# Kernel optimization log

Hardware: AMD Instinct MI355X
Metric: run time of the kernel (lower is better)

Reference implementation:

```python
import jax, jax.numpy as jnp
import numpy as np
import math

VOCAB = 32000
D_MODEL = 1024
N_HEADS = 16
D_FF = 4096
N_LAYERS = 4
MAX_LEN = 2048
BATCH = 2
SEQ = 1024


def _sinusoidal_pe(max_len, d_model):
    pos = np.arange(max_len, dtype=np.float32)[:, None]
    div = np.exp(np.arange(0, d_model, 2, dtype=np.float32) * (-math.log(10000.0) / d_model))
    pe = np.zeros((max_len, d_model), dtype=np.float32)
    pe[:, 0::2] = np.sin(pos * div)
    pe[:, 1::2] = np.cos(pos * div)
    return jnp.asarray(pe)


def setup_inputs() -> dict:
    key = jax.random.key(0)
    ks = jax.random.split(key, 16)
    std = 0.02
    L, d, ff, V = N_LAYERS, D_MODEL, D_FF, VOCAB
    inp = {
        "input_ids": jax.random.randint(ks[0], (BATCH, SEQ), 0, V, dtype=jnp.int32),
        "tok_emb": jax.random.normal(ks[1], (V, d), jnp.float32) * std,
        "pe": _sinusoidal_pe(MAX_LEN, d),
        "Wq": jax.random.normal(ks[2], (L, d, d), jnp.float32) * std,
        "Wk": jax.random.normal(ks[3], (L, d, d), jnp.float32) * std,
        "Wv": jax.random.normal(ks[4], (L, d, d), jnp.float32) * std,
        "Wo": jax.random.normal(ks[5], (L, d, d), jnp.float32) * std,
        "bo": jnp.zeros((L, d), jnp.float32),
        "W1": jax.random.normal(ks[6], (L, d, ff), jnp.float32) * std,
        "b1": jnp.zeros((L, ff), jnp.float32),
        "W2": jax.random.normal(ks[7], (L, ff, d), jnp.float32) * std,
        "b2": jnp.zeros((L, d), jnp.float32),
        "ln1_g": jnp.ones((L, d), jnp.float32),
        "ln1_b": jnp.zeros((L, d), jnp.float32),
        "ln2_g": jnp.ones((L, d), jnp.float32),
        "ln2_b": jnp.zeros((L, d), jnp.float32),
        "lnf_g": jnp.ones((d,), jnp.float32),
        "lnf_b": jnp.zeros((d,), jnp.float32),
        "Whead": jax.random.normal(ks[8], (V, d), jnp.float32) * std,
    }
    return inp


def _layernorm(x, g, b, eps=1e-5):
    mu = jnp.mean(x, axis=-1, keepdims=True)
    var = jnp.var(x, axis=-1, keepdims=True)
    return (x - mu) * jax.lax.rsqrt(var + eps) * g + b


def reference(input_ids, tok_emb, pe, Wq, Wk, Wv, Wo, bo, W1, b1, W2, b2,
              ln1_g, ln1_b, ln2_g, ln2_b, lnf_g, lnf_b, Whead):
    B, S = input_ids.shape
    d, H = D_MODEL, N_HEADS
    dk = d // H
    scale = math.sqrt(dk)

    x = tok_emb[input_ids] * math.sqrt(d) + pe[:S][None, :, :]  # [B,S,d]
    causal = jnp.tril(jnp.ones((S, S), dtype=bool))  # [S,S]

    for l in range(N_LAYERS):
        # --- attention sub-block (pre-LN) ---
        h = _layernorm(x, ln1_g[l], ln1_b[l])
        q = (h @ Wq[l]).reshape(B, S, H, dk).transpose(0, 2, 1, 3)  # [B,H,S,dk]
        k = (h @ Wk[l]).reshape(B, S, H, dk).transpose(0, 2, 1, 3)
        v = (h @ Wv[l]).reshape(B, S, H, dk).transpose(0, 2, 1, 3)
        scores = jnp.einsum('bhqd,bhkd->bhqk', q, k) / scale  # [B,H,S,S]
        scores = jnp.where(causal[None, None], scores, -1e9)
        attn = jax.nn.softmax(scores, axis=-1)
        ctx = jnp.einsum('bhqk,bhkd->bhqd', attn, v)  # [B,H,S,dk]
        ctx = ctx.transpose(0, 2, 1, 3).reshape(B, S, d)
        x = x + ctx @ Wo[l] + bo[l]
        # --- feed-forward sub-block ---
        h = _layernorm(x, ln2_g[l], ln2_b[l])
        x = x + jax.nn.relu(h @ W1[l] + b1[l]) @ W2[l] + b2[l]

    x = _layernorm(x, lnf_g, lnf_b)
    logits = x @ Whead.T  # [B,S,V]
    return logits
```

## Files before the change

### kernel.cpp

```cpp
#include <hip/hip_runtime.h>
#include <stdint.h>

typedef unsigned short u16;
typedef unsigned int   u32;

#define D_MODEL 1024
#define NHEADS  16
#define DKH     64
#define DFF     4096
#define NLAYERS 4
#define BATCH   2
#define SEQ     1024
#define NTOK    (BATCH*SEQ)
#define NVOCAB  32000
#define QKV_LD  3072

typedef __bf16 bf16x8 __attribute__((ext_vector_type(8)));
typedef float  f32x4  __attribute__((ext_vector_type(4)));
typedef u32    u32x4  __attribute__((ext_vector_type(4)));

static __device__ __forceinline__ u16 f2bf(float f){
    union { float f; u32 u; } v; v.f = f;
    return (u16)((v.u + 0x7fffu + ((v.u >> 16) & 1u)) >> 16);
}
static __device__ __forceinline__ u32 pk2(float lo, float hi){
    return (u32)f2bf(lo) | ((u32)f2bf(hi) << 16);
}
static __device__ __forceinline__ bf16x8 ldb8(const u16* p){
    return *reinterpret_cast<const bf16x8*>(p);
}
static __device__ __forceinline__ f32x4 mfma16(bf16x8 a, bf16x8 b, f32x4 c){
    return __builtin_amdgcn_mfma_f32_16x16x32_bf16(a, b, c, 0, 0, 0);
}
static __device__ __forceinline__ void gld16(const void* g, void* l){
    __builtin_amdgcn_global_load_lds((__attribute__((address_space(1))) u32*)g,
                                     (__attribute__((address_space(3))) u32*)l, 16, 0, 0);
}

__global__ __launch_bounds__(256) void k_embed(const int* __restrict__ ids,
        const float* __restrict__ tok, const float* __restrict__ pe,
        float* __restrict__ x){
    int t = blockIdx.x;
    int c = threadIdx.x * 4;
    int id = ids[t];
    int s = t & (SEQ - 1);
    float4 tv = *(const float4*)(tok + (size_t)id * D_MODEL + c);
    float4 pv = *(const float4*)(pe  + (size_t)s  * D_MODEL + c);
    float4 o;
    o.x = tv.x * 32.0f + pv.x;
    o.y = tv.y * 32.0f + pv.y;
    o.z = tv.z * 32.0f + pv.z;
    o.w = tv.w * 32.0f + pv.w;
    *(float4*)(x + (size_t)t * D_MODEL + c) = o;
}

__global__ __launch_bounds__(256) void k_ln(const float* __restrict__ x,
        const float* __restrict__ g, const float* __restrict__ b,
        u16* __restrict__ out){
    int t = blockIdx.x;
    int tid = threadIdx.x;
    float4 v = *(const float4*)(x + (size_t)t * D_MODEL + tid * 4);
    float s  = v.x + v.y + v.z + v.w;
    float ss = v.x*v.x + v.y*v.y + v.z*v.z + v.w*v.w;
    #pragma unroll
    for (int off = 1; off < 64; off <<= 1){
        s  += __shfl_xor(s, off);
        ss += __shfl_xor(ss, off);
    }
    __shared__ float rs[4], rss[4];
    int w = tid >> 6;
    if ((tid & 63) == 0){ rs[w] = s; rss[w] = ss; }
    __syncthreads();
    s  = rs[0] + rs[1] + rs[2] + rs[3];
    ss = rss[0] + rss[1] + rss[2] + rss[3];
    float mu  = s * (1.0f / D_MODEL);
    float var = ss * (1.0f / D_MODEL) - mu * mu;
    float rstd = rsqrtf(var + 1e-5f);
    float4 gg = *(const float4*)(g + tid * 4);
    float4 bb = *(const float4*)(b + tid * 4);
    uint2 pkv;
    pkv.x = pk2((v.x - mu) * rstd * gg.x + bb.x, (v.y - mu) * rstd * gg.y + bb.y);
    pkv.y = pk2((v.z - mu) * rstd * gg.z + bb.z, (v.w - mu) * rstd * gg.w + bb.w);
    *(uint2*)(out + (size_t)t * D_MODEL + tid * 4) = pkv;
}

__global__ __launch_bounds__(256) void k_ln_acc(float* __restrict__ x,
        const float* __restrict__ p0, const float* __restrict__ p1,
        const float* __restrict__ bias,
        const float* __restrict__ g, const float* __restrict__ b,
        u16* __restrict__ out){
    int t = blockIdx.x;
    int tid = threadIdx.x;
    size_t idx = (size_t)t * D_MODEL + tid * 4;
    float4 v  = *(const float4*)(x + idx);
    float4 a0 = *(const float4*)(p0 + idx);
    float4 a1 = *(const float4*)(p1 + idx);
    float4 bv = *(const float4*)(bias + tid * 4);
    v.x += a0.x + a1.x + bv.x;
    v.y += a0.y + a1.y + bv.y;
    v.z += a0.z + a1.z + bv.z;
    v.w += a0.w + a1.w + bv.w;
    *(float4*)(x + idx) = v;
    float s  = v.x + v.y + v.z + v.w;
    float ss = v.x*v.x + v.y*v.y + v.z*v.z + v.w*v.w;
    #pragma unroll
    for (int off = 1; off < 64; off <<= 1){
        s  += __shfl_xor(s, off);
        ss += __shfl_xor(ss, off);
    }
    __shared__ float rs[4], rss[4];
    int w = tid >> 6;
    if ((tid & 63) == 0){ rs[w] = s; rss[w] = ss; }
    __syncthreads();
    s  = rs[0] + rs[1] + rs[2] + rs[3];
    ss = rss[0] + rss[1] + rss[2] + rss[3];
    float mu  = s * (1.0f / D_MODEL);
    float var = ss * (1.0f / D_MODEL) - mu * mu;
    float rstd = rsqrtf(var + 1e-5f);
    float4 gg = *(const float4*)(g + tid * 4);
    float4 bb = *(const float4*)(b + tid * 4);
    uint2 pkv;
    pkv.x = pk2((v.x - mu) * rstd * gg.x + bb.x, (v.y - mu) * rstd * gg.y + bb.y);
    pkv.y = pk2((v.z - mu) * rstd * gg.z + bb.z, (v.w - mu) * rstd * gg.w + bb.w);
    *(uint2*)(out + idx) = pkv;
}

__global__ __launch_bounds__(256) void k_cast(const float* __restrict__ in,
        u16* __restrict__ out){
    size_t i = ((size_t)blockIdx.x * 256 + threadIdx.x) * 8;
    float4 a = *(const float4*)(in + i);
    float4 b = *(const float4*)(in + i + 4);
    u32x4 o;
    o.x = pk2(a.x, a.y); o.y = pk2(a.z, a.w);
    o.z = pk2(b.x, b.y); o.w = pk2(b.z, b.w);
    *(u32x4*)(out + i) = o;
}

__global__ __launch_bounds__(256) void k_tconv_fused(
        const float* __restrict__ Wq, const float* __restrict__ Wk,
        const float* __restrict__ Wv, const float* __restrict__ Wo,
        const float* __restrict__ W1, const float* __restrict__ W2,
        u16* __restrict__ wqkvT, u16* __restrict__ woT,
        u16* __restrict__ w1T,   u16* __restrict__ w2T){
    __shared__ float tile[32][33];
    const int id = blockIdx.x;
    const float* in; u16* outp; int R, C, bx, by;
    if (id < 4096){
        int wsel = id >> 10, t = id & 1023;
        bx = t & 31; by = t >> 5; R = 1024; C = 1024;
        in   = (wsel == 0) ? Wq : (wsel == 1) ? Wk : (wsel == 2) ? Wv : Wo;
        outp = (wsel < 3) ? wqkvT + wsel * 1024 * 1024 : woT;
    } else if (id < 8192){
        int t = id - 4096; bx = t & 127; by = t >> 7;
        R = 1024; C = 4096; in = W1; outp = w1T;
    } else {
        int t = id - 8192; bx = t & 31; by = t >> 5;
        R = 4096; C = 1024; in = W2; outp = w2T;
    }
    const int tx = threadIdx.x & 31, ty = threadIdx.x >> 5;
    #pragma unroll
    for (int i = 0; i < 4; i++){
        int r = by * 32 + ty + i * 8;
        tile[ty + i * 8][tx] = in[(size_t)r * C + bx * 32 + tx];
    }
    __syncthreads();
    #pragma unroll
    for (int i = 0; i < 4; i++){
        int c = bx * 32 + ty + i * 8;
        outp[(size_t)c * R + by * 32 + tx] = f2bf(tile[tx][ty + i * 8]);
    }
}

__global__ __launch_bounds__(256) void k_vt(const u16* __restrict__ qkv,
        u16* __restrict__ vt){
    __shared__ u16 tile[32][33];
    int sb = blockIdx.x;
    int yz = blockIdx.y;
    int db = yz & 1;
    int bh = yz >> 1;
    int b = bh >> 4, h = bh & 15;
    int tx = threadIdx.x & 31, ty = threadIdx.x >> 5;
    #pragma unroll
    for (int i = 0; i < 4; i++){
        int s = sb * 32 + ty + i * 8;
        tile[ty + i * 8][tx] = qkv[(size_t)(b * SEQ + s) * QKV_LD + 2048 + h * DKH + db * 32 + tx];
    }
    __syncthreads();
    #pragma unroll
    for (int i = 0; i < 4; i++){
        int dh = db * 32 + ty + i * 8;
        vt[(size_t)(bh * DKH + dh) * SEQ + sb * 32 + tx] = tile[tx][ty + i * 8];
    }
}

template<bool BIAS, bool RELU, bool OBF16, bool AXISM>
__global__ __launch_bounds__(256) void k_gemm(
    const u16* __restrict__ A, const u16* __restrict__ Bt,
    const float* __restrict__ bias,
    float* __restrict__ outF, u16* __restrict__ outH,
    int N, int Kfull, int NXT, int NMT, int NZ)
{
    __shared__ __align__(16) u16 As[128 * 32];
    __shared__ __align__(16) u16 Bs[128 * 32];
    const int bid = blockIdx.x;
    const int xcd = bid & 7;
    const int r   = bid >> 3;
    int m_t, n_t, z;
    if constexpr (AXISM) {
        const int mper = NMT >> 3;
        n_t = r % NXT;
        int r2 = r / NXT;
        z = r2 % NZ;
        m_t = xcd * mper + r2 / NZ;
    } else {
        const int nper = NXT >> 3;
        n_t = xcd * nper + r % nper;
        int r2 = r / nper;
        m_t = r2 % NMT;
        z = r2 / NMT;
    }
    const int m0 = m_t * 128;
    const int n0 = n_t * 128;
    const int Kz = Kfull / NZ;
    const int kbeg = z * Kz, kend = kbeg + Kz;

    const int tid  = threadIdx.x;
    const int lane = tid & 63;
    const int w    = tid >> 6;
    const int wr   = w >> 1, wc = w & 1;
    const int lrow = lane & 15, lkg = lane >> 4;
    const int srow = lane >> 2;
    const int scg  = (lane & 3) * 8;

    const u16* aS0 = A  + (size_t)(m0 + w * 32 + srow) * Kfull + scg;
    const u16* bS0 = Bt + (size_t)(n0 + w * 32 + srow) * Kfull + scg;
    u16* aD0 = As + w * 1024;
    u16* bD0 = Bs + w * 1024;

    f32x4 acc[4][4] = {};

    for (int k0 = kbeg; k0 < kend; k0 += 32) {
        gld16(aS0 + k0, aD0);
        gld16(aS0 + k0 + (size_t)16 * Kfull, aD0 + 512);
        gld16(bS0 + k0, bD0);
        gld16(bS0 + k0 + (size_t)16 * Kfull, bD0 + 512);
        __syncthreads();
        bf16x8 af[4], bfv[4];
        #pragma unroll
        for (int i = 0; i < 4; i++)
            af[i] = ldb8(As + (64 * wr + 16 * i + lrow) * 32 + 8 * lkg);
        #pragma unroll
        for (int j = 0; j < 4; j++)
            bfv[j] = ldb8(Bs + (64 * wc + 16 * j + lrow) * 32 + 8 * lkg);
        #pragma unroll
        for (int i = 0; i < 4; i++)
            #pragma unroll
            for (int j = 0; j < 4; j++)
                acc[i][j] = mfma16(af[i], bfv[j], acc[i][j]);
        __syncthreads();
    }

    float* outFz = outF;
    if (NZ > 1) outFz += (size_t)z * (NMT * 128) * N;

    #pragma unroll
    for (int i = 0; i < 4; i++){
        #pragma unroll
        for (int j = 0; j < 4; j++){
            const int c = n0 + 64 * wc + 16 * j + lrow;
            float bv = 0.0f;
            if constexpr (BIAS) bv = bias[c];
            #pragma unroll
            for (int e = 0; e < 4; e++){
                const int rr = m0 + 64 * wr + 16 * i + lkg * 4 + e;
                float vv = acc[i][j][e] + bv;
                if constexpr (RELU) vv = fmaxf(vv, 0.0f);
                const size_t idx = (size_t)rr * N + c;
                if constexpr (OBF16) outH[idx] = f2bf(vv);
                else                 outFz[idx] = vv;
            }
        }
    }
}

__global__ __launch_bounds__(512, 2) void k_gemm_head256(
    const u16* __restrict__ A, const u16* __restrict__ Bt,
    float* __restrict__ out)
{
    __shared__ __align__(16) u16 lds[65536];
    const int bid = blockIdx.x;
    const int swz = (bid & 7) * 125 + (bid >> 3);
    const int m0 = (swz >> 3) * 256;
    const int n0 = (swz & 7) * 256;

    const int tid  = threadIdx.x;
    const int w    = tid >> 6;
    const int lane = tid & 63;
    const int wr   = w >> 2, wc = w & 3;
    const int lrow = lane & 15, lkg = lane >> 4;

    const int srow = tid >> 3;
    const int ssw  = ((tid & 7) ^ (srow & 7)) * 8;
    const u16* aSrc0 = A  + (size_t)(m0 +   0 + srow) * D_MODEL + ssw;
    const u16* aSrc1 = A  + (size_t)(m0 +  64 + srow) * D_MODEL + ssw;
    const u16* aSrc2 = A  + (size_t)(m0 + 128 + srow) * D_MODEL + ssw;
    const u16* aSrc3 = A  + (size_t)(m0 + 192 + srow) * D_MODEL + ssw;
    const u16* bSrc0 = Bt + (size_t)(n0 +   0 + srow) * D_MODEL + ssw;
    const u16* bSrc1 = Bt + (size_t)(n0 +  64 + srow) * D_MODEL + ssw;
    const u16* bSrc2 = Bt + (size_t)(n0 + 128 + srow) * D_MODEL + ssw;
    const u16* bSrc3 = Bt + (size_t)(n0 + 192 + srow) * D_MODEL + ssw;

    const int sw0 = ((0 + lkg) ^ (lrow & 7)) * 8;
    const int sw1 = ((4 + lkg) ^ (lrow & 7)) * 8;
    const int aBase = (wr * 128 + lrow) * 64;
    const int bBase = (wc * 64  + lrow) * 64;

    f32x4 acc[8][4] = {};

    #define STAGE(s, st) do { \
        u16* ab_ = lds + (s) * 32768 + w * 512; \
        const int ko_ = (st) * 64; \
        gld16(aSrc0 + ko_, ab_);              \
        gld16(aSrc1 + ko_, ab_ + 4096);       \
        gld16(aSrc2 + ko_, ab_ + 8192);       \
        gld16(aSrc3 + ko_, ab_ + 12288);      \
        gld16(bSrc0 + ko_, ab_ + 16384);      \
        gld16(bSrc1 + ko_, ab_ + 20480);      \
        gld16(bSrc2 + ko_, ab_ + 24576);      \
        gld16(bSrc3 + ko_, ab_ + 28672);      \
    } while (0)

    STAGE(0, 0);
    STAGE(1, 1);
    asm volatile("s_waitcnt vmcnt(8)" ::: "memory");
    __builtin_amdgcn_s_barrier();
    __builtin_amdgcn_sched_barrier(0);

    const int NT = D_MODEL / 64;
    for (int t = 0; t < NT; ++t){
        const int s = t & 1;
        const u16* As = lds + s * 32768;
        const u16* Bs = As + 16384;

        bf16x8 af0[8], bf0[4];
        #pragma unroll
        for (int i = 0; i < 8; i++) af0[i] = ldb8(As + aBase + i * 1024 + sw0);
        #pragma unroll
        for (int j = 0; j < 4; j++) bf0[j] = ldb8(Bs + bBase + j * 1024 + sw0);
        __builtin_amdgcn_s_setprio(1);
        #pragma unroll
        for (int i = 0; i < 8; i++)
            #pragma unroll
            for (int j = 0; j < 4; j++)
                acc[i][j] = mfma16(af0[i], bf0[j], acc[i][j]);
        __builtin_amdgcn_s_setprio(0);

        bf16x8 af1[8], bf1[4];
        #pragma unroll
        for (int i = 0; i < 8; i++) af1[i] = ldb8(As + aBase + i * 1024 + sw1);
        #pragma unroll
        for (int j = 0; j < 4; j++) bf1[j] = ldb8(Bs + bBase + j * 1024 + sw1);
        asm volatile("s_waitcnt lgkmcnt(0)" ::: "memory");
        __builtin_amdgcn_sched_barrier(0);
        __builtin_amdgcn_s_barrier();
        __builtin_amdgcn_sched_barrier(0);

        STAGE(s, (t + 2 < NT) ? t + 2 : NT - 1);

        __builtin_amdgcn_s_setprio(1);
        #pragma unroll
        for (int i = 0; i < 8; i++)
            #pragma unroll
            for (int j = 0; j < 4; j++)
                acc[i][j] = mfma16(af1[i], bf1[j], acc[i][j]);
        __builtin_amdgcn_s_setprio(0);

        asm volatile("s_waitcnt vmcnt(8)" ::: "memory");
        __builtin_amdgcn_s_barrier();
        __builtin_amdgcn_sched_barrier(0);
    }
    #undef STAGE

    #pragma unroll
    for (int i = 0; i < 8; i++){
        const int m = m0 + wr * 128 + i * 16 + lkg * 4;
        #pragma unroll
        for (int j = 0; j < 4; j++){
            const int n = n0 + wc * 64 + j * 16 + lrow;
            float4 st;
            st.x = acc[i][j][0]; st.y = acc[i][j][1];
            st.z = acc[i][j][2]; st.w = acc[i][j][3];
            *(float4*)(out + (size_t)n * NVOCAB + m) = st;
        }
    }
}

__global__ __launch_bounds__(256) void k_attn(const u16* __restrict__ qkv,
        const u16* __restrict__ vt, u16* __restrict__ ctx){
    const int wid  = (blockIdx.x << 2) + (threadIdx.x >> 6);
    const int lane = threadIdx.x & 63;
    const int qt = wid & 63;
    const int h  = (wid >> 6) & 15;
    const int b  = wid >> 10;
    const int q0 = qt * 16;
    const int lrow = lane & 15, lkg = lane >> 4;

    __shared__ __align__(16) u16 plds_all[4][16][56];
    u16 (*plds)[56] = plds_all[threadIdx.x >> 6];

    const u16* qbase = qkv + (size_t)(b * SEQ + q0 + lrow) * QKV_LD + h * DKH + 8 * lkg;
    const bf16x8 qf0 = ldb8(qbase);
    const bf16x8 qf1 = ldb8(qbase + 32);

    float mr[4], lsum[4];
    f32x4 acc[4] = {};
    #pragma unroll
    for (int e = 0; e < 4; e++){ mr[e] = -1e30f; lsum[e] = 0.0f; }

    const int kbmax = (q0 + 15) >> 5;
    const u16* kbase  = qkv + (size_t)(b * SEQ) * QKV_LD + 1024 + h * DKH;
    const u16* vtbase = vt + (size_t)((b * NHEADS + h) * DKH) * SEQ;

    for (int kb = 0; kb <= kbmax; ++kb){
        const int kc = kb * 32;
        f32x4 s0 = {0.f, 0.f, 0.f, 0.f}, s1 = {0.f, 0.f, 0.f, 0.f};
        const u16* kp0 = kbase + (size_t)(kc + lrow) * QKV_LD + 8 * lkg;
        const u16* kp1 = kp0 + (size_t)16 * QKV_LD;
        s0 = mfma16(qf0, ldb8(kp0), s0);
        s0 = mfma16(qf1, ldb8(kp0 + 32), s0);
        s1 = mfma16(qf0, ldb8(kp1), s1);
        s1 = mfma16(qf1, ldb8(kp1 + 32), s1);

        float sv0[4], sv1[4];
        #pragma unroll
        for (int e = 0; e < 4; e++){
            const int row = q0 + lkg * 4 + e;
            float a0 = s0[e] * 0.125f, a1 = s1[e] * 0.125f;
            sv0[e] = (kc + lrow      > row) ? -1e30f : a0;
            sv1[e] = (kc + 16 + lrow > row) ? -1e30f : a1;
        }
        #pragma unroll
        for (int e = 0; e < 4; e++){
            float t = fmaxf(sv0[e], sv1[e]);
            t = fmaxf(t, __shfl_xor(t, 1));
            t = fmaxf(t, __shfl_xor(t, 2));
            t = fmaxf(t, __shfl_xor(t, 4));
            t = fmaxf(t, __shfl_xor(t, 8));
            const float mn = fmaxf(mr[e], t);
            const float al = __expf(mr[e] - mn);
            const float p0 = __expf(sv0[e] - mn);
            const float p1 = __expf(sv1[e] - mn);
            float rsum = p0 + p1;
            rsum += __shfl_xor(rsum, 1);
            rsum += __shfl_xor(rsum, 2);
            rsum += __shfl_xor(rsum, 4);
            rsum += __shfl_xor(rsum, 8);
            lsum[e] = lsum[e] * al + rsum;
            mr[e] = mn;
            #pragma unroll
            for (int nt = 0; nt < 4; nt++) acc[nt][e] *= al;
            plds[lkg * 4 + e][lrow]      = f2bf(p0);
            plds[lkg * 4 + e][16 + lrow] = f2bf(p1);
        }
        asm volatile("" ::: "memory");
        const bf16x8 pf = ldb8(&plds[lrow][8 * lkg]);
        #pragma unroll
        for (int nt = 0; nt < 4; nt++){
            const u16* vp = vtbase + (size_t)(16 * nt + lrow) * SEQ + kc + 8 * lkg;
            acc[nt] = mfma16(pf, ldb8(vp), acc[nt]);
        }
    }
    #pragma unroll
    for (int nt = 0; nt < 4; nt++){
        #pragma unroll
        for (int e = 0; e < 4; e++){
            const int r = q0 + lkg * 4 + e;
            ctx[(size_t)(b * SEQ + r) * D_MODEL + h * DKH + 16 * nt + lrow] =
                f2bf(acc[nt][e] / lsum[e]);
        }
    }
}

extern "C" void kernel_launch(void* const* d_in, const int* in_sizes, int n_in,
                              void* d_out, int out_size, void* d_ws, size_t ws_size,
                              hipStream_t stream){
    const int*   ids  = (const int*)  d_in[0];
    const float* tok  = (const float*)d_in[1];
    const float* pe   = (const float*)d_in[2];
    const float* Wq   = (const float*)d_in[3];
    const float* Wk   = (const float*)d_in[4];
    const float* Wv   = (const float*)d_in[5];
    const float* Wo   = (const float*)d_in[6];
    const float* bo   = (const float*)d_in[7];
    const float* W1   = (const float*)d_in[8];
    const float* b1   = (const float*)d_in[9];
    const float* W2   = (const float*)d_in[10];
    const float* b2   = (const float*)d_in[11];
    const float* ln1g = (const float*)d_in[12];
    const float* ln1b = (const float*)d_in[13];
    const float* ln2g = (const float*)d_in[14];
    const float* ln2b = (const float*)d_in[15];
    const float* lnfg = (const float*)d_in[16];
    const float* lnfb = (const float*)d_in[17];
    const float* Wh   = (const float*)d_in[18];
    float* out = (float*)d_out;

    char* ws = (char*)d_ws;
    size_t off = 0;
    auto alloc = [&](size_t bytes) -> void* {
        void* p = ws + off;
        off += (bytes + 255) & ~(size_t)255;
        return p;
    };
    float* x     = (float*)alloc((size_t)NTOK * D_MODEL * 4);
    u16*   hbuf  = (u16*)  alloc((size_t)NTOK * D_MODEL * 2);
    u16*   qkv   = (u16*)  alloc((size_t)NTOK * QKV_LD  * 2);
    u16*   vt    = (u16*)  alloc((size_t)NTOK * D_MODEL * 2);
    u16*   ctx   = (u16*)  alloc((size_t)NTOK * D_MODEL * 2);
    u16*   f1    = (u16*)  alloc((size_t)NTOK * DFF     * 2);
    float* pbuf  = (float*)alloc((size_t)2 * NTOK * D_MODEL * 4);
    u16*   wqkvT = (u16*)  alloc((size_t)QKV_LD * D_MODEL * 2);
    u16*   woT   = (u16*)  alloc((size_t)D_MODEL * D_MODEL * 2);
    u16*   w1T   = (u16*)  alloc((size_t)DFF * D_MODEL * 2);
    u16*   w2T   = (u16*)  alloc((size_t)D_MODEL * DFF * 2);
    u16*   whB   = (u16*)  alloc((size_t)NVOCAB * D_MODEL * 2);
    float* p1    = pbuf + (size_t)NTOK * D_MODEL;
    (void)ws_size; (void)in_sizes; (void)n_in; (void)out_size;

    k_embed<<<NTOK, 256, 0, stream>>>(ids, tok, pe, x);
    k_cast<<<(NVOCAB * D_MODEL) / (256 * 8), 256, 0, stream>>>(Wh, whB);

    for (int l = 0; l < NLAYERS; l++){
        const size_t wdd = (size_t)l * D_MODEL * D_MODEL;
        const size_t wdf = (size_t)l * D_MODEL * DFF;
        k_tconv_fused<<<12288, 256, 0, stream>>>(
            Wq + wdd, Wk + wdd, Wv + wdd, Wo + wdd, W1 + wdf, W2 + wdf,
            wqkvT, woT, w1T, w2T);

        if (l == 0)
            k_ln<<<NTOK, 256, 0, stream>>>(x, ln1g, ln1b, hbuf);
        else
            k_ln_acc<<<NTOK, 256, 0, stream>>>(x, pbuf, p1, b2 + (l - 1) * D_MODEL,
                ln1g + l * D_MODEL, ln1b + l * D_MODEL, hbuf);

        k_gemm<false, false, true, false><<<384, 256, 0, stream>>>(
            hbuf, wqkvT, nullptr, nullptr, qkv, QKV_LD, D_MODEL, 24, 16, 1);
        k_vt<<<dim3(32, 64), 256, 0, stream>>>(qkv, vt);
        k_attn<<<512, 256, 0, stream>>>(qkv, vt, ctx);

        k_gemm<false, false, false, true><<<256, 256, 0, stream>>>(
            ctx, woT, nullptr, pbuf, nullptr, D_MODEL, D_MODEL, 8, 16, 2);
        k_ln_acc<<<NTOK, 256, 0, stream>>>(x, pbuf, p1, bo + l * D_MODEL,
            ln2g + l * D_MODEL, ln2b + l * D_MODEL, hbuf);

        k_gemm<true, true, true, false><<<512, 256, 0, stream>>>(
            hbuf, w1T, b1 + l * DFF, nullptr, f1, DFF, D_MODEL, 32, 16, 1);
        k_gemm<false, false, false, true><<<256, 256, 0, stream>>>(
            f1, w2T, nullptr, pbuf, nullptr, D_MODEL, DFF, 8, 16, 2);
    }

    k_ln_acc<<<NTOK, 256, 0, stream>>>(x, pbuf, p1, b2 + 3 * D_MODEL,
        lnfg, lnfb, hbuf);
    k_gemm_head256<<<1000, 512, 0, stream>>>(whB, hbuf, out);
}
```

Baseline: 1.116 ms.

## Double-buffer GEMM LDS tiles with K=64 stages, XOR swizzle and async prefetch

Rewrites the layer GEMM main loop to use a 2-stage LDS ring of 128x64 A/B tiles, loaded by global-to-LDS copies issued two steps ahead, with vmcnt waits in place of full syncthreads after each load. LDS rows are XOR-swizzled to avoid bank conflicts on the fragment reads, and s_setprio raises priority around the MFMA bursts. The goal is to hide global load latency behind matrix math and halve the barrier count per K. It uses 64KB of LDS per block, which could limit occupancy even with the launch-bounds hint of 2 blocks.

```diff
diff --git a/kernel.cpp b/kernel.cpp
--- a/kernel.cpp
+++ b/kernel.cpp
@@ -194,14 +194,13 @@
 }
 
 template<bool BIAS, bool RELU, bool OBF16, bool AXISM>
-__global__ __launch_bounds__(256) void k_gemm(
+__global__ __launch_bounds__(256, 2) void k_gemm128p(
     const u16* __restrict__ A, const u16* __restrict__ Bt,
     const float* __restrict__ bias,
     float* __restrict__ outF, u16* __restrict__ outH,
     int N, int Kfull, int NXT, int NMT, int NZ)
 {
-    __shared__ __align__(16) u16 As[128 * 32];
-    __shared__ __align__(16) u16 Bs[128 * 32];
+    __shared__ __align__(16) u16 lds[32768];
     const int bid = blockIdx.x;
     const int xcd = bid & 7;
     const int r   = bid >> 3;
@@ -222,43 +221,94 @@
     const int m0 = m_t * 128;
     const int n0 = n_t * 128;
     const int Kz = Kfull / NZ;
-    const int kbeg = z * Kz, kend = kbeg + Kz;
+    const int kbeg = z * Kz;
+    const int NT = Kz >> 6;
 
     const int tid  = threadIdx.x;
+    const int w    = tid >> 6;
     const int lane = tid & 63;
-    const int w    = tid >> 6;
     const int wr   = w >> 1, wc = w & 1;
     const int lrow = lane & 15, lkg = lane >> 4;
-    const int srow = lane >> 2;
-    const int scg  = (lane & 3) * 8;
-
-    const u16* aS0 = A  + (size_t)(m0 + w * 32 + srow) * Kfull + scg;
-    const u16* bS0 = Bt + (size_t)(n0 + w * 32 + srow) * Kfull + scg;
-    u16* aD0 = As + w * 1024;
-    u16* bD0 = Bs + w * 1024;
+
+    const int srow = tid >> 3;
+    const int ssw  = ((tid & 7) ^ (srow & 7)) * 8;
+    const u16* aSrc0 = A  + (size_t)(m0 +  0 + srow) * Kfull + kbeg + ssw;
+    const u16* aSrc1 = A  + (size_t)(m0 + 32 + srow) * Kfull + kbeg + ssw;
+    const u16* aSrc2 = A  + (size_t)(m0 + 64 + srow) * Kfull + kbeg + ssw;
+    const u16* aSrc3 = A  + (size_t)(m0 + 96 + srow) * Kfull + kbeg + ssw;
+    const u16* bSrc0 = Bt + (size_t)(n0 +  0 + srow) * Kfull + kbeg + ssw;
+    const u16* bSrc1 = Bt + (size_t)(n0 + 32 + srow) * Kfull + kbeg + ssw;
+    const u16* bSrc2 = Bt + (size_t)(n0 + 64 + srow) * Kfull + kbeg + ssw;
+    const u16* bSrc3 = Bt + (size_t)(n0 + 96 + srow) * Kfull + kbeg + ssw;
+
+    const int sw0 = ((0 + lkg) ^ (lrow & 7)) * 8;
+    const int sw1 = ((4 + lkg) ^ (lrow & 7)) * 8;
+    const int aBase = (wr * 64 + lrow) * 64;
+    const int bBase = (wc * 64 + lrow) * 64 + 8192;
 
     f32x4 acc[4][4] = {};
 
-    for (int k0 = kbeg; k0 < kend; k0 += 32) {
-        gld16(aS0 + k0, aD0);
-        gld16(aS0 + k0 + (size_t)16 * Kfull, aD0 + 512);
-        gld16(bS0 + k0, bD0);
-        gld16(bS0 + k0 + (size_t)16 * Kfull, bD0 + 512);
-        __syncthreads();
-        bf16x8 af[4], bfv[4];
-        #pragma unroll
-        for (int i = 0; i < 4; i++)
-            af[i] = ldb8(As + (64 * wr + 16 * i + lrow) * 32 + 8 * lkg);
-        #pragma unroll
-        for (int j = 0; j < 4; j++)
-            bfv[j] = ldb8(Bs + (64 * wc + 16 * j + lrow) * 32 + 8 * lkg);
+    #define STAGE(s, st) do { \
+        u16* ab_ = lds + (s) * 16384 + w * 512; \
+        const int ko_ = (st) * 64; \
+        gld16(aSrc0 + ko_, ab_);              \
+        gld16(aSrc1 + ko_, ab_ + 2048);       \
+        gld16(aSrc2 + ko_, ab_ + 4096);       \
+        gld16(aSrc3 + ko_, ab_ + 6144);       \
+        gld16(bSrc0 + ko_, ab_ + 8192);       \
+        gld16(bSrc1 + ko_, ab_ + 10240);      \
+        gld16(bSrc2 + ko_, ab_ + 12288);      \
+        gld16(bSrc3 + ko_, ab_ + 14336);      \
+    } while (0)
+
+    STAGE(0, 0);
+    STAGE(1, 1);
+    asm volatile("s_waitcnt vmcnt(8)" ::: "memory");
+    __builtin_amdgcn_s_barrier();
+    __builtin_amdgcn_sched_barrier(0);
+
+    for (int t = 0; t < NT; ++t){
+        const int s = t & 1;
+        const u16* As = lds + s * 16384;
+
+        bf16x8 af0[4], bf0[4];
+        #pragma unroll
+        for (int i = 0; i < 4; i++) af0[i] = ldb8(As + aBase + i * 1024 + sw0);
+        #pragma unroll
+        for (int j = 0; j < 4; j++) bf0[j] = ldb8(As + bBase + j * 1024 + sw0);
+        __builtin_amdgcn_s_setprio(1);
         #pragma unroll
         for (int i = 0; i < 4; i++)
             #pragma unroll
             for (int j = 0; j < 4; j++)
-                acc[i][j] = mfma16(af[i], bfv[j], acc[i][j]);
-        __syncthreads();
-    }
+                acc[i][j] = mfma16(af0[i], bf0[j], acc[i][j]);
+        __builtin_amdgcn_s_setprio(0);
+
+        bf16x8 af1[4], bf1[4];
+        #pragma unroll
+        for (int i = 0; i < 4; i++) af1[i] = ldb8(As + aBase + i * 1024 + sw1);
+        #pragma unroll
+        for (int j = 0; j < 4; j++) bf1[j] = ldb8(As + bBase + j * 1024 + sw1);
+        asm volatile("s_waitcnt lgkmcnt(0)" ::: "memory");
+        __builtin_amdgcn_sched_barrier(0);
+        __builtin_amdgcn_s_barrier();
+        __builtin_amdgcn_sched_barrier(0);
+
+        STAGE(s, (t + 2 < NT) ? t + 2 : NT - 1);
+
+        __builtin_amdgcn_s_setprio(1);
+        #pragma unroll
+        for (int i = 0; i < 4; i++)
+            #pragma unroll
+            for (int j = 0; j < 4; j++)
+                acc[i][j] = mfma16(af1[i], bf1[j], acc[i][j]);
+        __builtin_amdgcn_s_setprio(0);
+
+        asm volatile("s_waitcnt vmcnt(8)" ::: "memory");
+        __builtin_amdgcn_s_barrier();
+        __builtin_amdgcn_sched_barrier(0);
+    }
+    #undef STAGE
 
     float* outFz = outF;
     if (NZ > 1) outFz += (size_t)z * (NMT * 128) * N;
@@ -543,19 +593,19 @@
             k_ln_acc<<<NTOK, 256, 0, stream>>>(x, pbuf, p1, b2 + (l - 1) * D_MODEL,
                 ln1g + l * D_MODEL, ln1b + l * D_MODEL, hbuf);
 
-        k_gemm<false, false, true, false><<<384, 256, 0, stream>>>(
+        k_gemm128p<false, false, true, false><<<384, 256, 0, stream>>>(
             hbuf, wqkvT, nullptr, nullptr, qkv, QKV_LD, D_MODEL, 24, 16, 1);
         k_vt<<<dim3(32, 64), 256, 0, stream>>>(qkv, vt);
         k_attn<<<512, 256, 0, stream>>>(qkv, vt, ctx);
 
-        k_gemm<false, false, false, true><<<256, 256, 0, stream>>>(
+        k_gemm128p<false, false, false, true><<<256, 256, 0, stream>>>(
             ctx, woT, nullptr, pbuf, nullptr, D_MODEL, D_MODEL, 8, 16, 2);
         k_ln_acc<<<NTOK, 256, 0, stream>>>(x, pbuf, p1, bo + l * D_MODEL,
             ln2g + l * D_MODEL, ln2b + l * D_MODEL, hbuf);
 
-        k_gemm<true, true, true, false><<<512, 256, 0, stream>>>(
+        k_gemm128p<true, true, true, false><<<512, 256, 0, stream>>>(
             hbuf, w1T, b1 + l * DFF, nullptr, f1, DFF, D_MODEL, 32, 16, 1);
-        k_gemm<false, false, false, true><<<256, 256, 0, stream>>>(
+        k_gemm128p<false, false, false, true><<<256, 256, 0, stream>>>(
             f1, w2T, nullptr, pbuf, nullptr, D_MODEL, DFF, 8, 16, 2);
     }
 
```

Result: faster. 939.9 us (-15.8%).
